# Kernel tuning notes

Measured on AMD Instinct MI355X. Metric: run time of the kernel, lower is better.

The kernel has to match this reference:

```python
import jax, jax.numpy as jnp
import numpy as np

HEADS = 4
DIM_K = 16
DIM_U = 1
EPS = 1e-5


def _rel_pos_idx(n):
    # torch: meshgrid(ij) -> stack -> '(i j) n'; rel = pos[None,:]-pos[:,None] + n-1
    ii, jj = np.meshgrid(np.arange(n), np.arange(n), indexing='ij')
    pos = np.stack([ii, jj]).reshape(2, -1).T  # (n*n, 2)
    rel = pos[None, :] - pos[:, None] + (n - 1)  # (N, N, 2)
    return rel[..., 0], rel[..., 1]


def _bn(t, gamma, beta):
    # BatchNorm2d in training mode: batch stats over (b, h, w), biased var
    mu = t.mean(axis=(0, 1, 2))
    var = t.var(axis=(0, 1, 2))
    return (t - mu) * jax.lax.rsqrt(var + EPS) * gamma + beta


def setup_inputs() -> dict:
    key = jax.random.key(0)
    ks = jax.random.split(key, 16)
    b, n, c = 8, 48, 128
    hk = DIM_K * HEADS          # 64
    v = 128 // HEADS            # 32 (dim_out // heads)
    rl = 2 * n - 1              # 95
    s = 0.02
    return {
        'x': jax.random.normal(ks[0], (b, n, n, c), jnp.float32),
        'cor': jax.random.normal(ks[1], (b, n, n, 2), jnp.float32),
        'Wq': jax.random.normal(ks[2], (hk, c), jnp.float32) * s,
        'Wk': jax.random.normal(ks[3], (DIM_K * DIM_U, c), jnp.float32) * s,
        'Wv': jax.random.normal(ks[4], (v * DIM_U, c), jnp.float32) * s,
        'Wce': jax.random.normal(ks[5], (hk, 2), jnp.float32) * s,
        'bce': jax.random.normal(ks[6], (hk,), jnp.float32) * s,
        'Wcc': jax.random.normal(ks[7], (hk, 128), jnp.float32) * s,
        'Wmp': jax.random.normal(ks[8], (128, hk), jnp.float32) * s,
        'bmp': jax.random.normal(ks[9], (128,), jnp.float32) * s,
        'gq': jnp.ones((hk,), jnp.float32),
        'bq': jnp.zeros((hk,), jnp.float32),
        'gv': jnp.ones((v * DIM_U,), jnp.float32),
        'bv': jnp.zeros((v * DIM_U,), jnp.float32),
        'rel_pos_emb': jax.random.normal(ks[10], (rl, rl, DIM_K, DIM_U), jnp.float32),
    }


def reference(x, cor, Wq, Wk, Wv, Wce, bce, Wcc, Wmp, bmp, gq, bq, gv, bv, rel_pos_emb):
    b, hh, ww, c = x.shape
    h, u, kd = HEADS, DIM_U, DIM_K
    vd = Wv.shape[0] // u
    N = hh * ww

    # frame reversal along batch
    x_rev = jnp.concatenate([x[b // 2:], x[:b // 2]], axis=0)

    # 1x1 convs as channel matmuls (channels-last)
    q = jnp.einsum('bhwc,oc->bhwo', x, Wq)
    k = jnp.einsum('bhwc,oc->bhwo', x_rev, Wk)
    v = jnp.einsum('bhwc,oc->bhwo', x_rev, Wv)

    Qn = _bn(q, gq, bq)
    Vn = _bn(v, gv, bv)

    Q = jnp.transpose(Qn.reshape(b, N, h, kd), (0, 2, 3, 1))       # b h k n
    K = jnp.transpose(k.reshape(b, N, u, kd), (0, 2, 3, 1))        # b u k m
    V = jnp.transpose(Vn.reshape(b, N, u, vd), (0, 2, 3, 1))       # b u v m

    K = jax.nn.softmax(K, axis=-1)
    lamc = jnp.einsum('bukm,buvm->bkv', K, V)
    Yc = jnp.einsum('bhkn,bkv->bhvn', Q, lamc)

    # relative position lambda (global branch)
    ni, mi = _rel_pos_idx(hh)
    emb = rel_pos_emb[ni, mi]                                      # n m k u
    lamp = jnp.einsum('nmku,buvm->bnkv', emb, V)
    Yp = jnp.einsum('bhkn,bnkv->bhvn', Q, lamp)

    Y = Yc + Yp                                                    # b h v n
    appearance = jnp.transpose(Y.reshape(b, h, vd, hh, ww), (0, 3, 4, 1, 2)).reshape(b, hh, ww, h * vd)

    cor_embed_ = jnp.einsum('bhwc,oc->bhwo', cor, Wce) + bce       # b hh ww (h k)
    cor_embed = jnp.transpose(cor_embed_.reshape(b, N, h, kd), (0, 2, 3, 1))  # b h k n
    crc = jnp.einsum('bhkn,bkv->bhvn', cor_embed, lamc)
    crp = jnp.einsum('bhkn,bnkv->bhvn', cor_embed, lamp)
    cor_reverse_ = jnp.transpose((crc + crp).reshape(b, h, vd, hh, ww), (0, 3, 4, 1, 2)).reshape(b, hh, ww, h * vd)
    cor_reverse = jnp.einsum('bhwc,oc->bhwo', cor_reverse_, Wcc)
    motion = jnp.einsum('bhwc,oc->bhwo', cor_reverse - cor_embed_, Wmp) + bmp
    return appearance, motion
```

## Files before the change

kernel.cpp:

```cpp
#include <hip/hip_runtime.h>
#include <math.h>

#define NNPOS 2304
#define ROWS  18432
#define NK    96

#define O_Q   0ul
#define O_K   1179648ul
#define O_V   1474560ul
#define O_ST  2064384ul
#define O_VP  2064704ul
#define O_QP  2457920ul
#define O_CE  4817216ul
#define O_LC  5996864ul
#define O_CR  6000960ul
#define O_RT  8360256ul
#define O_WG  8450368ul
#define O_B2  8450624ul
#define O_WB  8450752ul
#define O_PT  8457920ul
#define O_PV  8466112ul
#define O_PE  8468160ul
#define O_WFB 8469184ul

typedef __bf16 bf16x8 __attribute__((ext_vector_type(8)));
typedef float  f32x4  __attribute__((ext_vector_type(4)));
typedef unsigned int u32;
typedef u32 u32x4 __attribute__((ext_vector_type(4)));

__global__ void k_fold(const float* __restrict__ Wcc, const float* __restrict__ Wce,
                       const float* __restrict__ Wmp, const float* __restrict__ bmp,
                       const float* __restrict__ bce, const float* __restrict__ Wq,
                       const float* __restrict__ Wk, const float* __restrict__ Wv,
                       float* __restrict__ ws) {
  const int t = threadIdx.x;
  const int g = blockIdx.x * 256 + t;
  const int o2 = g >> 7, c = g & 127;
  float acc = 0.f;
#pragma unroll 8
  for (int o = 0; o < 64; ++o) acc += Wmp[o2 * 64 + o] * Wcc[o * 128 + c];
  ((__bf16*)(ws + O_WFB))[o2 * 128 + c] = (__bf16)acc;
  if (blockIdx.x == 0 && t < 128) {
    float a0 = 0.f, a1 = 0.f, ab = 0.f;
#pragma unroll 8
    for (int o = 0; o < 64; ++o) {
      float w = Wmp[t * 64 + o];
      a0 += w * Wce[o * 2]; a1 += w * Wce[o * 2 + 1]; ab += w * bce[o];
    }
    ws[O_WG + t * 2] = a0; ws[O_WG + t * 2 + 1] = a1; ws[O_B2 + t] = bmp[t] - ab;
  }
  __bf16* wbp = (__bf16*)(ws + O_WB);
  if (g < 14336) {
    float w;
    if (g < 8192) w = Wq[g];
    else if (g < 10240) w = Wk[g - 8192];
    else w = Wv[g - 10240];
    wbp[g] = (__bf16)w;
  }
}

__global__ __launch_bounds__(256) void k_qkv(const float* __restrict__ x,
                                             float* __restrict__ ws) {
  const int t = threadIdx.x;
  const int wave = t >> 6, lane = t & 63;
  const int lr = lane & 15, quad = lane >> 4;
  const int r0 = blockIdx.x * 64 + wave * 16;
  const int b = r0 / NNPOS;
  const int n0 = r0 - b * NNPOS;
  const size_t outbase = (size_t)(((b + 4) & 7)) * NNPOS + n0;

  const __bf16* wb = (const __bf16*)(ws + O_WB);
  const float* xrow = x + (size_t)(r0 + lr) * 128;

  f32x4 acc[7];
#pragma unroll
  for (int i = 0; i < 7; ++i) acc[i] = (f32x4){0.f, 0.f, 0.f, 0.f};

#pragma unroll
  for (int ks = 0; ks < 4; ++ks) {
    const float* ap = xrow + ks * 32 + quad * 8;
    float4 a0 = *(const float4*)(ap);
    float4 a1 = *(const float4*)(ap + 4);
    bf16x8 af;
    af[0] = (__bf16)a0.x; af[1] = (__bf16)a0.y; af[2] = (__bf16)a0.z; af[3] = (__bf16)a0.w;
    af[4] = (__bf16)a1.x; af[5] = (__bf16)a1.y; af[6] = (__bf16)a1.z; af[7] = (__bf16)a1.w;
#pragma unroll
    for (int ct = 0; ct < 7; ++ct) {
      bf16x8 bfrag = *(const bf16x8*)(wb + (ct * 16 + lr) * 128 + ks * 32 + quad * 8);
      acc[ct] = __builtin_amdgcn_mfma_f32_16x16x32_bf16(af, bfrag, acc[ct], 0, 0, 0);
    }
  }

#pragma unroll
  for (int ct = 0; ct < 7; ++ct) {
#pragma unroll
    for (int reg = 0; reg < 4; ++reg) {
      int m = quad * 4 + reg;
      int oc = ct * 16 + lr;
      float vvv = acc[ct][reg];
      if (ct < 4)      ws[O_Q + (size_t)(r0 + m) * 64 + oc] = vvv;
      else if (ct < 5) ws[O_K + (outbase + m) * 16 + (oc - 64)] = vvv;
      else             ws[O_V + (outbase + m) * 32 + (oc - 80)] = vvv;
    }
  }
}

__global__ void k_rt(const float* __restrict__ rel, float* __restrict__ ws) {
  __bf16* rt = (__bf16*)(ws + O_RT);
  int i = blockIdx.x * 256 + threadIdx.x;
  if (i < 144400) {
    int kc = i & 15, rr = i >> 4;
    int ri = rr / 95, rj = rr - ri * 95;
    rt[(size_t)kc * 9216 + ri * 96 + rj] = (__bf16)rel[i];
  }
}

__global__ void k_zero(float* __restrict__ ws) {
  __bf16* vp = (__bf16*)(ws + O_VP);
  int i = blockIdx.x * 256 + threadIdx.x;
  if (i < 4096) ws[O_LC + i] = 0.f;
  int bv = i / 96, rem = i - bv * 96;
  int mi = rem >> 1, h8 = rem & 1;
  uint4 z; z.x = 0; z.y = 0; z.z = 0; z.w = 0;
  *(uint4*)(vp + (size_t)bv * 3072 + mi * 64 + 48 + h8 * 8) = z;
}

__global__ void k_stats1(float* __restrict__ ws) {
  const int t = threadIdx.x, blk = blockIdx.x;
  __shared__ float sh[512];
  if (blk < 64) {
    const int ch = t & 63, rsub = t >> 6;
    const float* src = ws + O_Q;
    const int r0 = blk * 288;
    float s = 0.f, s2 = 0.f;
#pragma unroll 4
    for (int i = 0; i < 72; ++i) {
      float v = src[(size_t)(r0 + rsub + i * 4) * 64 + ch];
      s += v; s2 += v * v;
    }
    sh[t] = s; sh[256 + t] = s2;
    __syncthreads();
    if (t < 64) {
      float S = sh[t] + sh[t + 64] + sh[t + 128] + sh[t + 192];
      float S2 = sh[256 + t] + sh[256 + t + 64] + sh[256 + t + 128] + sh[256 + t + 192];
      ws[O_PT + blk * 128 + t * 2] = S; ws[O_PT + blk * 128 + t * 2 + 1] = S2;
    }
  } else if (blk < 96) {
    const int j = blk - 64;
    const int ch = t & 31, rsub = t >> 5;
    const float* src = ws + O_V;
    const int r0 = j * 576;
    float s = 0.f, s2 = 0.f;
#pragma unroll 4
    for (int i = 0; i < 72; ++i) {
      float v = src[(size_t)(r0 + rsub + i * 8) * 32 + ch];
      s += v; s2 += v * v;
    }
    sh[t] = s; sh[256 + t] = s2;
    __syncthreads();
    if (t < 32) {
      float S = 0.f, S2 = 0.f;
#pragma unroll
      for (int k = 0; k < 8; ++k) { S += sh[t + k * 32]; S2 += sh[256 + t + k * 32]; }
      ws[O_PV + j * 64 + t * 2] = S; ws[O_PV + j * 64 + t * 2 + 1] = S2;
    }
  } else {
    const int idx = blk - 96;
    const int b = idx >> 3, sl = idx & 7;
    const int kc = t & 15, rsub = t >> 4;
    const int r0 = b * 2304 + sl * 288;
    float s = 0.f;
#pragma unroll 2
    for (int i = 0; i < 18; ++i)
      s += __expf(ws[O_K + (size_t)(r0 + rsub + i * 16) * 16 + kc]);
    sh[t] = s;
    __syncthreads();
    if (t < 16) {
      float S = 0.f;
#pragma unroll
      for (int k = 0; k < 16; ++k) S += sh[t + k * 16];
      ws[O_PE + b * 128 + sl * 16 + t] = S;
    }
  }
}

__global__ void k_stats2(const float* __restrict__ gq, const float* __restrict__ bq,
                         const float* __restrict__ gv, const float* __restrict__ bv,
                         float* __restrict__ ws) {
  const int t = threadIdx.x;
  if (t < 64) {
    float S = 0.f, S2 = 0.f;
    for (int i = 0; i < 64; ++i) { S += ws[O_PT + i * 128 + t * 2]; S2 += ws[O_PT + i * 128 + t * 2 + 1]; }
    float mu = S / 18432.f, var = S2 / 18432.f - mu * mu;
    float sc = gq[t] * rsqrtf(var + 1e-5f);
    ws[O_ST + t] = sc; ws[O_ST + 64 + t] = bq[t] - mu * sc;
  } else if (t < 96) {
    int ch = t - 64;
    float S = 0.f, S2 = 0.f;
    for (int i = 0; i < 32; ++i) { S += ws[O_PV + i * 64 + ch * 2]; S2 += ws[O_PV + i * 64 + ch * 2 + 1]; }
    float mu = S / 18432.f, var = S2 / 18432.f - mu * mu;
    float sc = gv[ch] * rsqrtf(var + 1e-5f);
    ws[O_ST + 128 + ch] = sc; ws[O_ST + 160 + ch] = bv[ch] - mu * sc;
  } else if (t < 224) {
    int idx = t - 96; int b = idx >> 4, kc = idx & 15;
    float S = 0.f;
#pragma unroll
    for (int sl = 0; sl < 8; ++sl) S += ws[O_PE + b * 128 + sl * 16 + kc];
    ws[O_ST + 192 + idx] = 1.f / S;
  }
}

__global__ void k_prep(const float* __restrict__ cor, const float* __restrict__ Wce,
                       const float* __restrict__ bce, float* __restrict__ ws) {
  const int t = threadIdx.x;
  const int rl = t >> 5, j = t & 31;
  const int rid = blockIdx.x * 8 + rl;
  const int b = rid / NNPOS, n = rid - b * NNPOS;
  const float* st = ws + O_ST;
  __bf16* vp = (__bf16*)(ws + O_VP);
  float vvn = ws[O_V + (size_t)rid * 32 + j] * st[128 + j] + st[160 + j];
  vp[(size_t)(b * 32 + j) * 3072 + (n / 48) * 64 + (n % 48)] = (__bf16)vvn;
  float c0 = cor[rid * 2], c1 = cor[rid * 2 + 1];
#pragma unroll
  for (int ch = j; ch < 64; ch += 32) {
    float qn = ws[O_Q + (size_t)rid * 64 + ch] * st[ch] + st[64 + ch];
    ws[O_QP + (size_t)(n * 8 + b) * 128 + ch] = qn;
    float ce = c0 * Wce[ch * 2] + c1 * Wce[ch * 2 + 1] + bce[ch];
    ws[O_QP + (size_t)(n * 8 + b) * 128 + 64 + ch] = ce;
  }
}

__global__ void k_lamc(float* __restrict__ ws) {
  const int b = blockIdx.x / 9, sl = blockIdx.x - b * 9;
  const int t = threadIdx.x;
  __shared__ float eK[16][16];
  __shared__ float Vn[16][33];
  const float* st = ws + O_ST;
  const int kc = t & 15, vp_ = t >> 4;
  const int v0 = vp_ * 2, v1 = v0 + 1;
  float a0 = 0.f, a1 = 0.f;
  const int m0 = b * 2304 + sl * 256;
  const int jj = t & 31, rw = t >> 5;
  const float scj = st[128 + jj], bij = st[160 + jj];
  for (int ch = 0; ch < 16; ++ch) {
    const int mbase = m0 + ch * 16;
    eK[t >> 4][t & 15] = __expf(ws[O_K + (size_t)(mbase + (t >> 4)) * 16 + (t & 15)]);
    Vn[rw][jj]     = ws[O_V + (size_t)(mbase + rw) * 32 + jj] * scj + bij;
    Vn[rw + 8][jj] = ws[O_V + (size_t)(mbase + rw + 8) * 32 + jj] * scj + bij;
    __syncthreads();
#pragma unroll
    for (int m = 0; m < 16; ++m) {
      float e = eK[m][kc];
      a0 += e * Vn[m][v0];
      a1 += e * Vn[m][v1];
    }
    __syncthreads();
  }
  atomicAdd(&ws[O_LC + (size_t)(b * 16 + kc) * 32 + v0], a0);
  atomicAdd(&ws[O_LC + (size_t)(b * 16 + kc) * 32 + v1], a1);
}

__global__ __launch_bounds__(256, 2) void k_lamp(float* __restrict__ ws,
                                                 float* __restrict__ out) {
  __shared__ __align__(16) char smem[33792];
  bf16x8* Bs16 = (bf16x8*)smem;
  u32* Sw = (u32*)(smem + 8192);
  float* Cs = (float*)smem;

  const int t = threadIdx.x;
  const int bx = blockIdx.x;
  const int ni = bx / 6;
  const int sset = bx - ni * 6;
  const int s0 = (sset < 3) ? sset * 16 : (sset - 3) * 16 + 1;
  const int chalf = blockIdx.y;
  const int colbase = chalf * 128;
  const int wave = t >> 6, lane = t & 63;
  const int wrow = wave >> 1, wcol = wave & 1;
  const int lr = lane & 15, quad = lane >> 4;

  const __bf16* vp = (const __bf16*)(ws + O_VP);
  const unsigned short* rp = (const unsigned short*)(ws + O_RT);

  const int ia0 = t;
  const int kcA0 = ia0 / 24, wpA0 = ia0 - kcA0 * 24;
  const int ia1 = t + 256;
  const int kcA1 = ia1 / 24, wpA1 = ia1 - kcA1 * 24;
  const bool hasA1 = (ia1 < 384);

  const int colB0 = t >> 2, pB0 = ((t & 3) - ((t >> 3) & 3)) & 3;
  const int ub1 = t + 256;
  const int colB1 = ub1 >> 2, pB1 = ((ub1 & 3) - ((ub1 >> 3) & 3)) & 3;
  const __bf16* gB0 = vp + (size_t)(colbase + colB0) * 3072 + pB0 * 8;
  const __bf16* gB1 = vp + (size_t)(colbase + colB1) * 3072 + pB1 * 8;

  f32x4 acc[4][4];
  {
    f32x4 zz = {0.f, 0.f, 0.f, 0.f};
#pragma unroll
    for (int i = 0; i < 4; ++i)
#pragma unroll
      for (int j = 0; j < 4; ++j) acc[i][j] = zz;
  }

  u32 sa[2] = {0, 0}, sb[2] = {0, 0};
  bf16x8 vA[2], vB[2];

  auto loadStep = [&](int ksn, u32& sA_, u32& sB_, bf16x8& v0_, bf16x8& v1_) {
    const int mi = ksn >> 1, mj0 = (ksn & 1) << 5;
    const int P0 = 96 * (mi - ni + 47) + mj0 - s0 + 33;
    const int k0 = ksn * 32;
    long b0 = (long)kcA0 * 9216 + P0 + 2 * wpA0;
    if (P0 & 1) sA_ = (u32)rp[b0] | ((u32)rp[b0 + 1] << 16);
    else        sA_ = *(const u32*)(rp + b0);
    if (hasA1) {
      long b1 = (long)kcA1 * 9216 + P0 + 2 * wpA1;
      if (P0 & 1) sB_ = (u32)rp[b1] | ((u32)rp[b1 + 1] << 16);
      else        sB_ = *(const u32*)(rp + b1);
    }
    v0_ = *(const bf16x8*)(gB0 + k0);
    v1_ = *(const bf16x8*)(gB1 + k0);
  };

  loadStep(0, sa[0], sb[0], vA[0], vB[0]);
  loadStep(1, sa[1], sb[1], vA[1], vB[1]);

  auto step = [&](int ks, u32& sA_, u32& sB_, bf16x8& v0_, bf16x8& v1_) {
    __syncthreads();
    Sw[kcA0 * 25 + wpA0] = sA_;
    if (hasA1) Sw[kcA1 * 25 + wpA1] = sB_;
    Bs16[t] = v0_;
    Bs16[t + 256] = v1_;
    __syncthreads();
    if (ks + 2 < NK) loadStep(ks + 2, sA_, sB_, v0_, v1_);

    bf16x8 af[4], bfr[4];
#pragma unroll
    for (int rt = 0; rt < 4; ++rt) {
      int nl = wrow * 4 + rt;
      int wb = lr * 25 + (7 - nl) + quad * 4;
      u32x4 dd = { Sw[wb], Sw[wb + 1], Sw[wb + 2], Sw[wb + 3] };
      af[rt] = __builtin_bit_cast(bf16x8, dd);
    }
#pragma unroll
    for (int ct = 0; ct < 4; ++ct) {
      int col = wcol * 64 + ct * 16 + lr;
      int u = col * 4 + ((quad + (col >> 1)) & 3);
      bfr[ct] = Bs16[u];
    }
#pragma unroll
    for (int rt = 0; rt < 4; ++rt)
#pragma unroll
      for (int ct = 0; ct < 4; ++ct)
        acc[rt][ct] = __builtin_amdgcn_mfma_f32_16x16x32_bf16(af[rt], bfr[ct], acc[rt][ct], 0, 0, 0);
  };

  for (int ks2 = 0; ks2 < NK; ks2 += 2) {
    step(ks2,     sa[0], sb[0], vA[0], vB[0]);
    step(ks2 + 1, sa[1], sb[1], vA[1], vB[1]);
  }

  const float* lamc = ws + O_LC;
  const float* Qp = ws + O_QP;
  __bf16* CRb = (__bf16*)(ws + O_CR);
  const int s = t >> 5, vv = t & 31;

  for (int h = 0; h < 2; ++h) {
    __syncthreads();
    if (wrow == h) {
#pragma unroll
      for (int rt = 0; rt < 4; ++rt) {
#pragma unroll
        for (int ct = 0; ct < 4; ++ct) {
          int col = wcol * 64 + ct * 16 + lr;
          int bb = chalf * 4 + (col >> 5);
          int vl = col & 31;
#pragma unroll
          for (int reg = 0; reg < 4; ++reg) {
            int row = rt * 16 + quad * 4 + reg;
            int kc = row & 15;
            float dinv = ws[O_ST + 192 + bb * 16 + kc];
            Cs[row * 132 + col] = acc[rt][ct][reg] + lamc[(bb * 16 + kc) * 32 + vl] * dinv;
          }
        }
      }
    }
    __syncthreads();
#pragma unroll
    for (int i = 0; i < 16; ++i) {
      int combo = s * 16 + i;
      int hp = combo & 7, bl = (combo >> 3) & 3, nr = combo >> 5;
      int n = ni * 48 + s0 + 2 * (h * 4 + nr);
      int bb = chalf * 4 + bl;
      const float* qrow = Qp + ((size_t)(n * 8 + bb) * 8 + hp) * 16;
      const float* crow = Cs + (nr * 16) * 132 + bl * 32 + vv;
      float y = 0.f;
#pragma unroll
      for (int kc = 0; kc < 16; ++kc) y += qrow[kc] * crow[kc * 132];
      size_t idx = (size_t)(bb * NNPOS + n) * 128 + (hp & 3) * 32 + vv;
      if (hp < 4) out[idx] = y;
      else        CRb[idx] = (__bf16)y;
    }
  }
}

__global__ __launch_bounds__(256) void k_motion(const float* __restrict__ cor,
                                                float* __restrict__ ws,
                                                float* __restrict__ out) {
  const int t = threadIdx.x;
  const int wave = t >> 6, lane = t & 63;
  const int lr = lane & 15, quad = lane >> 4;
  const int r0 = blockIdx.x * 64 + wave * 16;
  const __bf16* crb = (const __bf16*)(ws + O_CR);
  const __bf16* wfb = (const __bf16*)(ws + O_WFB);

  f32x4 acc[8];
#pragma unroll
  for (int i = 0; i < 8; ++i) acc[i] = (f32x4){0.f, 0.f, 0.f, 0.f};

#pragma unroll
  for (int ks = 0; ks < 4; ++ks) {
    bf16x8 af = *(const bf16x8*)(crb + (size_t)(r0 + lr) * 128 + ks * 32 + quad * 8);
#pragma unroll
    for (int ct = 0; ct < 8; ++ct) {
      bf16x8 bfrag = *(const bf16x8*)(wfb + (ct * 16 + lr) * 128 + ks * 32 + quad * 8);
      acc[ct] = __builtin_amdgcn_mfma_f32_16x16x32_bf16(af, bfrag, acc[ct], 0, 0, 0);
    }
  }

#pragma unroll
  for (int reg = 0; reg < 4; ++reg) {
    int row = r0 + quad * 4 + reg;
    float c0 = cor[row * 2], c1 = cor[row * 2 + 1];
#pragma unroll
    for (int ct = 0; ct < 8; ++ct) {
      int o2 = ct * 16 + lr;
      float y = acc[ct][reg] + ws[O_B2 + o2] - c0 * ws[O_WG + o2 * 2] - c1 * ws[O_WG + o2 * 2 + 1];
      out[2359296ul + (size_t)row * 128 + o2] = y;
    }
  }
}

extern "C" void kernel_launch(void* const* d_in, const int* in_sizes, int n_in,
                              void* d_out, int out_size, void* d_ws, size_t ws_size,
                              hipStream_t stream) {
  const float* x   = (const float*)d_in[0];
  const float* cor = (const float*)d_in[1];
  const float* Wq  = (const float*)d_in[2];
  const float* Wk  = (const float*)d_in[3];
  const float* Wv  = (const float*)d_in[4];
  const float* Wce = (const float*)d_in[5];
  const float* bce = (const float*)d_in[6];
  const float* Wcc = (const float*)d_in[7];
  const float* Wmp = (const float*)d_in[8];
  const float* bmp = (const float*)d_in[9];
  const float* gq  = (const float*)d_in[10];
  const float* bq  = (const float*)d_in[11];
  const float* gv  = (const float*)d_in[12];
  const float* bv  = (const float*)d_in[13];
  const float* rel = (const float*)d_in[14];
  float* out = (float*)d_out;
  float* ws  = (float*)d_ws;

  k_fold  <<<64, 256, 0, stream>>>(Wcc, Wce, Wmp, bmp, bce, Wq, Wk, Wv, ws);
  k_qkv   <<<288, 256, 0, stream>>>(x, ws);
  k_rt    <<<565, 256, 0, stream>>>(rel, ws);
  k_zero  <<<96, 256, 0, stream>>>(ws);
  k_stats1<<<160, 256, 0, stream>>>(ws);
  k_stats2<<<1, 256, 0, stream>>>(gq, bq, gv, bv, ws);
  k_lamc  <<<72, 256, 0, stream>>>(ws);
  k_prep  <<<2304, 256, 0, stream>>>(cor, Wce, bce, ws);
  k_lamp  <<<dim3(288, 2), 256, 0, stream>>>(ws, out);
  k_motion<<<288, 256, 0, stream>>>(cor, ws, out);
}
```

Baseline: 261.2 us.

## Load lamp A-fragments directly from parity-shifted rel table; split V packing kernel

Two copies of the bf16 relative-position table are now built, one shifted by one element, so the lamp GEMM can read its Toeplitz A fragments straight from global memory as aligned 8-element loads instead of staging them through shared memory. The lamp kernel shrinks to 128-thread blocks with 64 output columns, a 4-wide grid and double-buffered B tiles in LDS. V packing moves out of k_prep into a new k_vp kernel that transposes through shared memory and writes packed words, and k_lamc gets four times as many blocks. In exchange there is extra table memory, one more launch, and redundant global reads of A per wave instead of shared reuse.

After: 298.5 us. 14.3% more time.

```diff
diff --git a/kernel.cpp b/kernel.cpp
--- a/kernel.cpp
+++ b/kernel.cpp
@@ -11,22 +11,21 @@
 #define O_ST  2064384ul
 #define O_VP  2064704ul
 #define O_QP  2457920ul
-#define O_CE  4817216ul
-#define O_LC  5996864ul
-#define O_CR  6000960ul
-#define O_RT  8360256ul
-#define O_WG  8450368ul
-#define O_B2  8450624ul
-#define O_WB  8450752ul
-#define O_PT  8457920ul
-#define O_PV  8466112ul
-#define O_PE  8468160ul
-#define O_WFB 8469184ul
+#define O_LC  4817216ul
+#define O_CR  4821312ul
+#define O_RT  6000960ul
+#define O_WG  6148416ul
+#define O_B2  6148672ul
+#define O_WB  6148800ul
+#define O_PT  6155968ul
+#define O_PV  6164160ul
+#define O_PE  6166208ul
+#define O_WFB 6167232ul
 
 typedef __bf16 bf16x8 __attribute__((ext_vector_type(8)));
 typedef float  f32x4  __attribute__((ext_vector_type(4)));
 typedef unsigned int u32;
-typedef u32 u32x4 __attribute__((ext_vector_type(4)));
+struct __attribute__((packed, aligned(4))) bf16x8p { bf16x8 v; };
 
 __global__ void k_fold(const float* __restrict__ Wcc, const float* __restrict__ Wce,
                        const float* __restrict__ Wmp, const float* __restrict__ bmp,
@@ -111,7 +110,10 @@
   if (i < 144400) {
     int kc = i & 15, rr = i >> 4;
     int ri = rr / 95, rj = rr - ri * 95;
-    rt[(size_t)kc * 9216 + ri * 96 + rj] = (__bf16)rel[i];
+    int d = ri * 96 + rj;
+    __bf16 v = (__bf16)rel[i];
+    rt[(size_t)kc * 9216 + d] = v;
+    if (d > 0) rt[147456ul + (size_t)kc * 9216 + d - 1] = v;
   }
 }
 
@@ -210,6 +212,31 @@
   }
 }
 
+__global__ void k_vp(float* __restrict__ ws) {
+  const int b = blockIdx.x / 48, mi = blockIdx.x - b * 48;
+  const int t = threadIdx.x;
+  __shared__ float Vn[48 * 33];
+  const float* st = ws + O_ST;
+  const int r0 = b * 2304 + mi * 48;
+#pragma unroll
+  for (int i = t; i < 1536; i += 256) {
+    int r = i >> 5, j = i & 31;
+    Vn[r * 33 + j] = ws[O_V + (size_t)(r0 + r) * 32 + j] * st[128 + j] + st[160 + j];
+  }
+  __syncthreads();
+  __bf16* vp = (__bf16*)(ws + O_VP);
+  const int j = t >> 3, seg = t & 7;
+  unsigned short u[6];
+#pragma unroll
+  for (int q = 0; q < 6; ++q)
+    u[q] = __builtin_bit_cast(unsigned short, (__bf16)Vn[(seg * 6 + q) * 33 + j]);
+  u32 w0 = (u32)u[0] | ((u32)u[1] << 16);
+  u32 w1 = (u32)u[2] | ((u32)u[3] << 16);
+  u32 w2 = (u32)u[4] | ((u32)u[5] << 16);
+  u32* dst = (u32*)(vp + (size_t)(b * 32 + j) * 3072 + mi * 64 + seg * 6);
+  dst[0] = w0; dst[1] = w1; dst[2] = w2;
+}
+
 __global__ void k_prep(const float* __restrict__ cor, const float* __restrict__ Wce,
                        const float* __restrict__ bce, float* __restrict__ ws) {
   const int t = threadIdx.x;
@@ -217,9 +244,6 @@
   const int rid = blockIdx.x * 8 + rl;
   const int b = rid / NNPOS, n = rid - b * NNPOS;
   const float* st = ws + O_ST;
-  __bf16* vp = (__bf16*)(ws + O_VP);
-  float vvn = ws[O_V + (size_t)rid * 32 + j] * st[128 + j] + st[160 + j];
-  vp[(size_t)(b * 32 + j) * 3072 + (n / 48) * 64 + (n % 48)] = (__bf16)vvn;
   float c0 = cor[rid * 2], c1 = cor[rid * 2 + 1];
 #pragma unroll
   for (int ch = j; ch < 64; ch += 32) {
@@ -231,7 +255,7 @@
 }
 
 __global__ void k_lamc(float* __restrict__ ws) {
-  const int b = blockIdx.x / 9, sl = blockIdx.x - b * 9;
+  const int b = blockIdx.x / 36, sl = blockIdx.x - b * 36;
   const int t = threadIdx.x;
   __shared__ float eK[16][16];
   __shared__ float Vn[16][33];
@@ -239,10 +263,10 @@
   const int kc = t & 15, vp_ = t >> 4;
   const int v0 = vp_ * 2, v1 = v0 + 1;
   float a0 = 0.f, a1 = 0.f;
-  const int m0 = b * 2304 + sl * 256;
+  const int m0 = b * 2304 + sl * 64;
   const int jj = t & 31, rw = t >> 5;
   const float scj = st[128 + jj], bij = st[160 + jj];
-  for (int ch = 0; ch < 16; ++ch) {
+  for (int ch = 0; ch < 4; ++ch) {
     const int mbase = m0 + ch * 16;
     eK[t >> 4][t & 15] = __expf(ws[O_K + (size_t)(mbase + (t >> 4)) * 16 + (t & 15)]);
     Vn[rw][jj]     = ws[O_V + (size_t)(mbase + rw) * 32 + jj] * scj + bij;
@@ -260,11 +284,10 @@
   atomicAdd(&ws[O_LC + (size_t)(b * 16 + kc) * 32 + v1], a1);
 }
 
-__global__ __launch_bounds__(256, 2) void k_lamp(float* __restrict__ ws,
+__global__ __launch_bounds__(128, 3) void k_lamp(float* __restrict__ ws,
                                                  float* __restrict__ out) {
-  __shared__ __align__(16) char smem[33792];
+  __shared__ __align__(16) char smem[17408];
   bf16x8* Bs16 = (bf16x8*)smem;
-  u32* Sw = (u32*)(smem + 8192);
   float* Cs = (float*)smem;
 
   const int t = threadIdx.x;
@@ -272,26 +295,23 @@
   const int ni = bx / 6;
   const int sset = bx - ni * 6;
   const int s0 = (sset < 3) ? sset * 16 : (sset - 3) * 16 + 1;
-  const int chalf = blockIdx.y;
-  const int colbase = chalf * 128;
-  const int wave = t >> 6, lane = t & 63;
-  const int wrow = wave >> 1, wcol = wave & 1;
+  const int by = blockIdx.y;
+  const int colbase = by * 64;
+  const int w = t >> 6, lane = t & 63;
   const int lr = lane & 15, quad = lane >> 4;
 
   const __bf16* vp = (const __bf16*)(ws + O_VP);
-  const unsigned short* rp = (const unsigned short*)(ws + O_RT);
-
-  const int ia0 = t;
-  const int kcA0 = ia0 / 24, wpA0 = ia0 - kcA0 * 24;
-  const int ia1 = t + 256;
-  const int kcA1 = ia1 / 24, wpA1 = ia1 - kcA1 * 24;
-  const bool hasA1 = (ia1 < 384);
-
-  const int colB0 = t >> 2, pB0 = ((t & 3) - ((t >> 3) & 3)) & 3;
-  const int ub1 = t + 256;
-  const int colB1 = ub1 >> 2, pB1 = ((ub1 & 3) - ((ub1 >> 3) & 3)) & 3;
-  const __bf16* gB0 = vp + (size_t)(colbase + colB0) * 3072 + pB0 * 8;
-  const __bf16* gB1 = vp + (size_t)(colbase + colB1) * 3072 + pB1 * 8;
+  const __bf16* rtb = (const __bf16*)(ws + O_RT);
+
+  const int u0 = t, u1 = t + 128;
+  const int c0 = u0 >> 2, p0 = ((u0 & 3) - (c0 >> 1)) & 3;
+  const int c1 = u1 >> 2, p1 = ((u1 & 3) - (c1 >> 1)) & 3;
+  const __bf16* gB0 = vp + (size_t)(colbase + c0) * 3072 + p0 * 8;
+  const __bf16* gB1 = vp + (size_t)(colbase + c1) * 3072 + p1 * 8;
+
+  const int parity = (s0 + 1) & 1;
+  const __bf16* baseA = rtb + (size_t)parity * 147456 +
+                        (size_t)lr * 9216 + quad * 8 - 2 * (w * 4);
 
   f32x4 acc[4][4];
   {
@@ -302,84 +322,75 @@
       for (int j = 0; j < 4; ++j) acc[i][j] = zz;
   }
 
-  u32 sa[2] = {0, 0}, sb[2] = {0, 0};
-  bf16x8 vA[2], vB[2];
-
-  auto loadStep = [&](int ksn, u32& sA_, u32& sB_, bf16x8& v0_, bf16x8& v1_) {
-    const int mi = ksn >> 1, mj0 = (ksn & 1) << 5;
-    const int P0 = 96 * (mi - ni + 47) + mj0 - s0 + 33;
-    const int k0 = ksn * 32;
-    long b0 = (long)kcA0 * 9216 + P0 + 2 * wpA0;
-    if (P0 & 1) sA_ = (u32)rp[b0] | ((u32)rp[b0 + 1] << 16);
-    else        sA_ = *(const u32*)(rp + b0);
-    if (hasA1) {
-      long b1 = (long)kcA1 * 9216 + P0 + 2 * wpA1;
-      if (P0 & 1) sB_ = (u32)rp[b1] | ((u32)rp[b1 + 1] << 16);
-      else        sB_ = *(const u32*)(rp + b1);
-    }
-    v0_ = *(const bf16x8*)(gB0 + k0);
-    v1_ = *(const bf16x8*)(gB1 + k0);
+  bf16x8 afA[4], afB[4], vb0, vb1;
+
+  auto loadA = [&](int ksn, bf16x8* dst) {
+    int mi = ksn >> 1, mj0 = (ksn & 1) << 5;
+    const __bf16* p = baseA + (96 * (mi - ni + 47) + mj0 - s0 + 47 - parity);
+#pragma unroll
+    for (int rt = 0; rt < 4; ++rt)
+      dst[rt] = ((const bf16x8p*)(p - 2 * rt))->v;
   };
-
-  loadStep(0, sa[0], sb[0], vA[0], vB[0]);
-  loadStep(1, sa[1], sb[1], vA[1], vB[1]);
-
-  auto step = [&](int ks, u32& sA_, u32& sB_, bf16x8& v0_, bf16x8& v1_) {
-    __syncthreads();
-    Sw[kcA0 * 25 + wpA0] = sA_;
-    if (hasA1) Sw[kcA1 * 25 + wpA1] = sB_;
-    Bs16[t] = v0_;
-    Bs16[t + 256] = v1_;
-    __syncthreads();
-    if (ks + 2 < NK) loadStep(ks + 2, sA_, sB_, v0_, v1_);
-
-    bf16x8 af[4], bfr[4];
-#pragma unroll
-    for (int rt = 0; rt < 4; ++rt) {
-      int nl = wrow * 4 + rt;
-      int wb = lr * 25 + (7 - nl) + quad * 4;
-      u32x4 dd = { Sw[wb], Sw[wb + 1], Sw[wb + 2], Sw[wb + 3] };
-      af[rt] = __builtin_bit_cast(bf16x8, dd);
-    }
+  auto loadB = [&](int ksn) {
+    int k0 = ksn * 32;
+    vb0 = *(const bf16x8*)(gB0 + k0);
+    vb1 = *(const bf16x8*)(gB1 + k0);
+  };
+
+  loadB(0);
+  Bs16[u0] = vb0; Bs16[u1] = vb1;
+  loadA(0, afA);
+  loadB(1);
+  __syncthreads();
+
+  for (int ks = 0; ks < NK; ks += 2) {
+    Bs16[256 + u0] = vb0; Bs16[256 + u1] = vb1;
+    loadB(ks + 2 < NK ? ks + 2 : NK - 1);
+    loadA(ks + 1, afB);
 #pragma unroll
     for (int ct = 0; ct < 4; ++ct) {
-      int col = wcol * 64 + ct * 16 + lr;
-      int u = col * 4 + ((quad + (col >> 1)) & 3);
-      bfr[ct] = Bs16[u];
-    }
-#pragma unroll
-    for (int rt = 0; rt < 4; ++rt)
-#pragma unroll
-      for (int ct = 0; ct < 4; ++ct)
-        acc[rt][ct] = __builtin_amdgcn_mfma_f32_16x16x32_bf16(af[rt], bfr[ct], acc[rt][ct], 0, 0, 0);
-  };
-
-  for (int ks2 = 0; ks2 < NK; ks2 += 2) {
-    step(ks2,     sa[0], sb[0], vA[0], vB[0]);
-    step(ks2 + 1, sa[1], sb[1], vA[1], vB[1]);
-  }
-
-  const float* lamc = ws + O_LC;
+      int col = ct * 16 + lr;
+      bf16x8 bfr = Bs16[col * 4 + ((quad + (col >> 1)) & 3)];
+#pragma unroll
+      for (int rt = 0; rt < 4; ++rt)
+        acc[rt][ct] = __builtin_amdgcn_mfma_f32_16x16x32_bf16(afA[rt], bfr, acc[rt][ct], 0, 0, 0);
+    }
+    __syncthreads();
+    Bs16[u0] = vb0; Bs16[u1] = vb1;
+    loadB(ks + 3 < NK ? ks + 3 : NK - 1);
+    if (ks + 2 < NK) loadA(ks + 2, afA);
+#pragma unroll
+    for (int ct = 0; ct < 4; ++ct) {
+      int col = ct * 16 + lr;
+      bf16x8 bfr = Bs16[256 + col * 4 + ((quad + (col >> 1)) & 3)];
+#pragma unroll
+      for (int rt = 0; rt < 4; ++rt)
+        acc[rt][ct] = __builtin_amdgcn_mfma_f32_16x16x32_bf16(afB[rt], bfr, acc[rt][ct], 0, 0, 0);
+    }
+    __syncthreads();
+  }
+
+  const float* lamcp = ws + O_LC;
   const float* Qp = ws + O_QP;
   __bf16* CRb = (__bf16*)(ws + O_CR);
   const int s = t >> 5, vv = t & 31;
 
   for (int h = 0; h < 2; ++h) {
     __syncthreads();
-    if (wrow == h) {
+    if (w == h) {
 #pragma unroll
       for (int rt = 0; rt < 4; ++rt) {
 #pragma unroll
         for (int ct = 0; ct < 4; ++ct) {
-          int col = wcol * 64 + ct * 16 + lr;
-          int bb = chalf * 4 + (col >> 5);
+          int col = ct * 16 + lr;
+          int bb = by * 2 + (col >> 5);
           int vl = col & 31;
 #pragma unroll
           for (int reg = 0; reg < 4; ++reg) {
             int row = rt * 16 + quad * 4 + reg;
             int kc = row & 15;
             float dinv = ws[O_ST + 192 + bb * 16 + kc];
-            Cs[row * 132 + col] = acc[rt][ct][reg] + lamc[(bb * 16 + kc) * 32 + vl] * dinv;
+            Cs[row * 68 + col] = acc[rt][ct][reg] + lamcp[(bb * 16 + kc) * 32 + vl] * dinv;
           }
         }
       }
@@ -388,14 +399,14 @@
 #pragma unroll
     for (int i = 0; i < 16; ++i) {
       int combo = s * 16 + i;
-      int hp = combo & 7, bl = (combo >> 3) & 3, nr = combo >> 5;
+      int hp = combo & 7, bl = (combo >> 3) & 1, nr = combo >> 4;
       int n = ni * 48 + s0 + 2 * (h * 4 + nr);
-      int bb = chalf * 4 + bl;
+      int bb = by * 2 + bl;
       const float* qrow = Qp + ((size_t)(n * 8 + bb) * 8 + hp) * 16;
-      const float* crow = Cs + (nr * 16) * 132 + bl * 32 + vv;
+      const float* crow = Cs + (nr * 16) * 68 + bl * 32 + vv;
       float y = 0.f;
 #pragma unroll
-      for (int kc = 0; kc < 16; ++kc) y += qrow[kc] * crow[kc * 132];
+      for (int kc = 0; kc < 16; ++kc) y += qrow[kc] * crow[kc * 68];
       size_t idx = (size_t)(bb * NNPOS + n) * 128 + (hp & 3) * 32 + vv;
       if (hp < 4) out[idx] = y;
       else        CRb[idx] = (__bf16)y;
@@ -467,8 +478,9 @@
   k_zero  <<<96, 256, 0, stream>>>(ws);
   k_stats1<<<160, 256, 0, stream>>>(ws);
   k_stats2<<<1, 256, 0, stream>>>(gq, bq, gv, bv, ws);
-  k_lamc  <<<72, 256, 0, stream>>>(ws);
+  k_vp    <<<384, 256, 0, stream>>>(ws);
+  k_lamc  <<<288, 256, 0, stream>>>(ws);
   k_prep  <<<2304, 256, 0, stream>>>(cor, Wce, bce, ws);
-  k_lamp  <<<dim3(288, 2), 256, 0, stream>>>(ws, out);
+  k_lamp  <<<dim3(288, 4), 128, 0, stream>>>(ws, out);
   k_motion<<<288, 256, 0, stream>>>(cor, ws, out);
 }
```
